# Optimization experiments

Hardware: AMD Instinct MI355X
Metric: run time of the kernel (lower is better)

The kernel has to match this reference:

```python
import jax, jax.numpy as jnp
import numpy as np

N_E = 16384
E_DIM = 256


def setup_inputs() -> dict:
    key = jax.random.key(0)
    k1, k2 = jax.random.split(key)
    z = jax.random.normal(k1, (16, E_DIM, 32, 32), dtype=jnp.float32)
    # nn.Embedding init: uniform(-1/n_e, 1/n_e)
    embedding_weight = jax.random.uniform(
        k2, (N_E, E_DIM), dtype=jnp.float32, minval=-1.0 / N_E, maxval=1.0 / N_E
    )
    return {"z": z, "embedding_weight": embedding_weight}


def reference(z, embedding_weight):
    # b c h w -> b h w c, flatten to (N, e_dim)
    zf = jnp.transpose(z, (0, 2, 3, 1)).reshape(-1, E_DIM)  # [N, d]
    # squared euclidean distances: ||z||^2 + ||e||^2 - 2 z.e^T
    d = (
        jnp.sum(zf ** 2, axis=1, keepdims=True)          # [N, 1]
        + jnp.sum(embedding_weight ** 2, axis=1)         # [n_e]
        - 2.0 * jnp.einsum("bd,nd->bn", zf, embedding_weight)  # [N, n_e]
    )
    min_encoding_indices = jnp.argmin(d, axis=1)  # [N] int
    return min_encoding_indices
```

## Files before the change

kernel.cpp:

```cpp
#include <hip/hip_runtime.h>

#define EDIM 256
#define NROW 16384
#define NCODE 16384
#define NBN 128
#define MARGIN 2.0e-4f

typedef _Float16 f16x8 __attribute__((ext_vector_type(8)));
typedef float f32x4 __attribute__((ext_vector_type(4)));

__device__ __forceinline__ void gll16(const void* g, void* l) {
  __builtin_amdgcn_global_load_lds((const __attribute__((address_space(1))) void*)g,
                                   (__attribute__((address_space(3))) void*)l, 16, 0, 0);
}
__device__ __forceinline__ void gll4(const void* g, void* l) {
  __builtin_amdgcn_global_load_lds((const __attribute__((address_space(1))) void*)g,
                                   (__attribute__((address_space(3))) void*)l, 4, 0, 0);
}

__global__ __launch_bounds__(256) void k_es(const float* __restrict__ e,
                                            float* __restrict__ es) {
  const int row = blockIdx.x * 4 + (threadIdx.x >> 6);
  const int lane = threadIdx.x & 63;
  float4 v = *(const float4*)&e[row * EDIM + lane * 4];
  double s = (double)v.x * v.x + (double)v.y * v.y + (double)v.z * v.z + (double)v.w * v.w;
#pragma unroll
  for (int off = 32; off > 0; off >>= 1) s += __shfl_down(s, off, 64);
  if (lane == 0) es[row] = (float)s;
}

__global__ __launch_bounds__(256) void k_cvt_e(const float* __restrict__ e,
                                               _Float16* __restrict__ Eh) {
  const int n = blockIdx.x;
  Eh[n * EDIM + threadIdx.x] = (_Float16)(e[n * EDIM + threadIdx.x] * 1024.0f);
}

__global__ __launch_bounds__(256) void k_cvt_z(const float* __restrict__ z,
                                               _Float16* __restrict__ Zh) {
  __shared__ float zl[EDIM * 64];
  const int t = threadIdx.x;
  const int rb = blockIdx.x;
  const int bb = rb >> 4;
  const int hw0 = (rb & 15) << 6;
  const float* zbase = z + (size_t)bb * EDIM * 1024 + hw0;
#pragma unroll 4
  for (int rep = 0; rep < 64; ++rep) {
    int c = rep * 4 + (t >> 6);
    zl[c * 64 + (t & 63)] = zbase[(size_t)c * 1024 + (t & 63)];
  }
  __syncthreads();
  const int mloc = t >> 2, part = t & 3;
#pragma unroll
  for (int i = 0; i < 8; ++i) {
    int c0 = part * 64 + i * 8;
    f16x8 v;
#pragma unroll
    for (int j = 0; j < 8; ++j) v[j] = (_Float16)zl[(c0 + j) * 64 + mloc];
    *(f16x8*)&Zh[(size_t)(rb * 64 + mloc) * EDIM + c0] = v;
  }
}

__global__ __launch_bounds__(256, 2) void k_gemm(const _Float16* __restrict__ Zh,
                                                 const _Float16* __restrict__ Eh,
                                                 float* __restrict__ lmin,
                                                 uint4* __restrict__ masks) {
  __shared__ __align__(16) char smem[32768];

  const int tid = threadIdx.x;
  const int lane = tid & 63;
  const int wv = tid >> 6;
  const int wm = wv & 1, wn = wv >> 1;
  const int fr = lane & 15;
  const int fq = lane >> 4;

  const int bid = (int)blockIdx.x;
  const int wgid = (bid & 7) * 2048 + (bid >> 3);
  const int st = wgid >> 8, wi = wgid & 255;
  const int bm = ((st & 7) << 4) | (wi & 15);
  const int bn = ((st >> 3) << 4) | (wi >> 4);

  const char* zh_b = (const char*)Zh;
  const char* eh_b = (const char*)Eh;

  auto stage = [&](int buf, int s) {
#pragma unroll
    for (int i = 0; i < 2; ++i) {
      const int L = (i * 256 + tid) * 16;
      const int row = L >> 6, kb = L & 63;
      gll16(zh_b + (size_t)(bm * 128 + row) * 512 + s * 64 + kb,
            smem + buf * 8192 + L);
      gll16(eh_b + (size_t)(bn * 128 + row) * 512 + s * 64 + kb,
            smem + 16384 + buf * 8192 + L);
    }
  };

  f32x4 acc[4][4];
#pragma unroll
  for (int i = 0; i < 4; ++i)
#pragma unroll
    for (int j = 0; j < 4; ++j) acc[i][j] = (f32x4)0.0f;

  stage(0, 0);
  __syncthreads();
#pragma unroll 1
  for (int s = 0; s < 8; ++s) {
    if (s + 1 < 8) stage((s + 1) & 1, s + 1);
    const char* aB = smem + (s & 1) * 8192;
    const char* bB = smem + 16384 + (s & 1) * 8192;
    f16x8 af[4], bf[4];
#pragma unroll
    for (int mi = 0; mi < 4; ++mi)
      af[mi] = *(const f16x8*)(aB + (wm * 64 + mi * 16 + fr) * 64 + fq * 16);
#pragma unroll
    for (int ni = 0; ni < 4; ++ni)
      bf[ni] = *(const f16x8*)(bB + (wn * 64 + ni * 16 + fr) * 64 + fq * 16);
#pragma unroll
    for (int mi = 0; mi < 4; ++mi)
#pragma unroll
      for (int ni = 0; ni < 4; ++ni)
        acc[mi][ni] = __builtin_amdgcn_mfma_f32_16x16x32_f16(af[mi], bf[ni], acc[mi][ni], 0, 0, 0);
    __syncthreads();
  }

  float* rowsmin = (float*)smem;
  float* rowminC = (float*)(smem + 1024);
  unsigned* msk = (unsigned*)(smem + 1536);
  msk[tid] = 0;
  msk[tid + 256] = 0;
  const float sc = -0.001953125f;
#pragma unroll
  for (int mi = 0; mi < 4; ++mi)
#pragma unroll
    for (int r = 0; r < 4; ++r) {
      float v = acc[mi][0][r] * sc;
      v = fminf(v, acc[mi][1][r] * sc);
      v = fminf(v, acc[mi][2][r] * sc);
      v = fminf(v, acc[mi][3][r] * sc);
#pragma unroll
      for (int off = 1; off < 16; off <<= 1) v = fminf(v, __shfl_xor(v, off, 64));
      if (fr == 0) rowsmin[(wm * 64 + mi * 16 + fq * 4 + r) * 2 + wn] = v;
    }
  __syncthreads();
  if (tid < 128) {
    float rm = fminf(rowsmin[tid * 2], rowsmin[tid * 2 + 1]);
    rowminC[tid] = rm;
    lmin[(size_t)bn * NROW + bm * 128 + tid] = rm;
  }
  __syncthreads();
#pragma unroll
  for (int mi = 0; mi < 4; ++mi)
#pragma unroll
    for (int r = 0; r < 4; ++r) {
      const int row = wm * 64 + mi * 16 + fq * 4 + r;
      const float thr = rowminC[row] + MARGIN;
#pragma unroll
      for (int ni = 0; ni < 4; ++ni) {
        if (acc[mi][ni][r] * sc <= thr) {
          const int col = wn * 64 + ni * 16 + fr;
          atomicOr(&msk[row * 4 + (col >> 5)], 1u << (col & 31));
        }
      }
    }
  __syncthreads();
  if (tid < 128) masks[(size_t)bn * NROW + bm * 128 + tid] = *(const uint4*)&msk[tid * 4];
}

__global__ __launch_bounds__(256) void k_rescore(const float* __restrict__ z,
                                                 const float* __restrict__ e,
                                                 const float* __restrict__ es,
                                                 const float* __restrict__ lmin,
                                                 const uint4* __restrict__ masks,
                                                 int* __restrict__ out) {
  extern __shared__ float zl[];
  float* lmin_s = zl + EDIM * 64;
  const int t = threadIdx.x;
  const int rb = (int)blockIdx.x;
  const int bb = rb >> 4;
  const int hw0 = (rb & 15) << 6;
  const int r0 = rb * 64;
  const float* zbase = z + (size_t)bb * EDIM * 1024 + hw0;
#pragma unroll 4
  for (int rep = 0; rep < 64; ++rep) {
    int c = rep * 4 + (t >> 6);
    zl[c * 64 + (t & 63)] = zbase[(size_t)c * 1024 + (t & 63)];
  }
#pragma unroll 4
  for (int i = 0; i < 32; ++i) {
    int bn = i * 4 + (t >> 6);
    lmin_s[bn * 64 + (t & 63)] = lmin[(size_t)bn * NROW + r0 + (t & 63)];
  }
  __syncthreads();

  const int r = t >> 2, q = t & 3;
  const int row = r0 + r;

  double sq = 0.0;
  {
    const float* zq = zl + (q * 64) * 64 + r;
    for (int k = 0; k < 64; ++k) {
      float v = zq[k * 64];
      sq = fma((double)v, (double)v, sq);
    }
  }
  double s01 = sq + __shfl_xor(sq, 1, 64);
  double zsd = s01 + __shfl_xor(s01, 2, 64);
  const float zs = (float)zsd;

  float g = 3.402823466e+38f;
#pragma unroll 8
  for (int j = 0; j < 32; ++j) g = fminf(g, lmin_s[(q * 32 + j) * 64 + r]);
  g = fminf(g, __shfl_xor(g, 1, 64));
  g = fminf(g, __shfl_xor(g, 2, 64));
  const float thr = g + MARGIN;

  float bestd = 3.402823466e+38f;
  int besti = 0x7fffffff;
#pragma unroll 1
  for (int j = 0; j < 32; ++j) {
    const int bn = q * 32 + j;
    if (lmin_s[bn * 64 + r] <= thr) {
      uint4 mk = masks[(size_t)bn * NROW + row];
      unsigned w[4] = {mk.x, mk.y, mk.z, mk.w};
#pragma unroll 1
      for (int qq = 0; qq < 4; ++qq) {
        unsigned u = w[qq];
        while (u) {
          int b = __ffs(u) - 1;
          u &= u - 1;
          const int code = bn * 128 + qq * 32 + b;
          const float* ep = e + (size_t)code * EDIM;
          float dot = 0.0f;
          for (int k = 0; k < EDIM; k += 4) {
            float4 ev = *(const float4*)(ep + k);
            dot = fmaf(zl[(k + 0) * 64 + r], ev.x, dot);
            dot = fmaf(zl[(k + 1) * 64 + r], ev.y, dot);
            dot = fmaf(zl[(k + 2) * 64 + r], ev.z, dot);
            dot = fmaf(zl[(k + 3) * 64 + r], ev.w, dot);
          }
          float d = (zs + es[code]) - 2.0f * dot;
          if (d < bestd) {
            bestd = d;
            besti = code;
          }
        }
      }
    }
  }
#pragma unroll
  for (int off = 1; off <= 2; off <<= 1) {
    float ov = __shfl_xor(bestd, off, 64);
    int oi = __shfl_xor(besti, off, 64);
    if (ov < bestd || (ov == bestd && oi < besti)) {
      bestd = ov;
      besti = oi;
    }
  }
  if (q == 0) out[row] = besti;
}

__global__ __launch_bounds__(256) void k_merge(const float* __restrict__ candv,
                                               const int* __restrict__ candi,
                                               int* __restrict__ out) {
  int n = blockIdx.x * 256 + threadIdx.x;
  float v0 = candv[n], v1 = candv[NROW + n];
  int i0 = candi[n], i1 = candi[NROW + n];
  out[n] = (v1 < v0) ? i1 : i0;
}

template <int SPLIT>
__global__ __launch_bounds__(256, 2) void k_main_fb(const float* __restrict__ z,
                                                    const float* __restrict__ e,
                                                    const float* __restrict__ es,
                                                    float* __restrict__ candv,
                                                    int* __restrict__ candi,
                                                    int* __restrict__ outd) {
  extern __shared__ char smemc[];
  float* As = (float*)smemc;
  float* Bs = (float*)(smemc + 16384);
  double* zred = (double*)(smemc + 16384 + 32768);
  float* zsf = (float*)(smemc + 16384 + 32768 + 2048);
  const int tid = threadIdx.x;
  const int lane = tid & 63;
  const int wv = tid >> 6;
  const int tm = tid & 7;
  const int tn = tid >> 3;
  const int rt = (int)blockIdx.x / SPLIT;
  const int sp = (int)blockIdx.x % SPLIT;
  const int bb = rt >> 4;
  const int hw0 = (rt & 15) << 6;
  const float* zb = z + bb * (EDIM * 1024) + hw0;
  const int codeBase = sp * (NCODE / SPLIT);
  const int NSTEP = (NCODE / SPLIT) / 256 * 8;
  auto stageA = [&](int buf, int gts) {
    const int k0 = (gts & 7) * 32;
    const float* g0 = zb + (size_t)k0 * 1024 + lane;
    float* l0 = As + buf * 2048 + (wv * 8) * 64;
#pragma unroll
    for (int s = 0; s < 8; ++s) gll4(g0 + (size_t)(wv * 8 + s) * 1024, l0 + s * 64);
  };
  float4 bpre[8];
  auto loadB = [&](int gts) {
    const int ct = gts >> 3, k0 = (gts & 7) * 32;
    const float* g = e + (size_t)(codeBase + ct * 256 + tid) * 256 + k0;
#pragma unroll
    for (int s = 0; s < 8; ++s) bpre[s] = *(const float4*)(g + s * 4);
  };
  auto writeB = [&](int buf) {
    float* bw_ = Bs + buf * 8192 + tid;
#pragma unroll
    for (int s = 0; s < 8; ++s) {
      bw_[(4 * s + 0) * 256] = bpre[s].x;
      bw_[(4 * s + 1) * 256] = bpre[s].y;
      bw_[(4 * s + 2) * 256] = bpre[s].z;
      bw_[(4 * s + 3) * 256] = bpre[s].w;
    }
  };
  stageA(0, 0);
  loadB(0);
  {
    const int m = tid & 63, qt = tid >> 6;
    const float* zp = zb + (size_t)(qt * 64) * 1024 + m;
    double s = 0.0;
    for (int k = 0; k < 64; ++k) {
      float v = zp[(size_t)k * 1024];
      s = fma((double)v, (double)v, s);
    }
    zred[qt * 64 + m] = s;
  }
  writeB(0);
  __syncthreads();
  if (tid < 64) {
    double sz = (zred[tid] + zred[64 + tid]) + (zred[128 + tid] + zred[192 + tid]);
    zsf[tid] = (float)sz;
  }
  __syncthreads();
  float zsr[8];
#pragma unroll
  for (int i = 0; i < 8; ++i) zsr[i] = zsf[tm * 8 + i];
  __syncthreads();
  float bestv[8];
  int besti[8];
#pragma unroll
  for (int i = 0; i < 8; ++i) {
    bestv[i] = 3.402823466e+38f;
    besti[i] = 0;
  }
  float acc[8][8];
  int cur = 0;
#pragma unroll 1
  for (int step = 0; step < NSTEP; ++step) {
    const int kc = step & 7, ct = step >> 3;
    if (step + 1 < NSTEP) {
      stageA(cur ^ 1, step + 1);
      loadB(step + 1);
    }
    if (kc == 0) {
#pragma unroll
      for (int i = 0; i < 8; ++i)
#pragma unroll
        for (int j = 0; j < 8; ++j) acc[i][j] = 0.0f;
    }
    const float* ak = As + cur * 2048 + tm * 8;
    const float* bk = Bs + cur * 8192 + tn * 8;
#pragma unroll 4
    for (int k = 0; k < 32; ++k) {
      float4 a0 = *(const float4*)(ak + k * 64);
      float4 a1 = *(const float4*)(ak + k * 64 + 4);
      float4 b0 = *(const float4*)(bk + k * 256);
      float4 b1 = *(const float4*)(bk + k * 256 + 4);
      float av[8] = {a0.x, a0.y, a0.z, a0.w, a1.x, a1.y, a1.z, a1.w};
      float bw[8] = {b0.x, b0.y, b0.z, b0.w, b1.x, b1.y, b1.z, b1.w};
#pragma unroll
      for (int i = 0; i < 8; ++i)
#pragma unroll
        for (int j = 0; j < 8; ++j) acc[i][j] = fmaf(av[i], bw[j], acc[i][j]);
    }
    if (step + 1 < NSTEP) writeB(cur ^ 1);
    if (kc == 7) {
      const int cb = codeBase + ct * 256 + tn * 8;
#pragma unroll
      for (int j = 0; j < 8; ++j) {
        float ej = es[cb + j];
#pragma unroll
        for (int i = 0; i < 8; ++i) {
          float d = (zsr[i] + ej) - 2.0f * acc[i][j];
          if (d < bestv[i]) {
            bestv[i] = d;
            besti[i] = cb + j;
          }
        }
      }
    }
    __syncthreads();
    cur ^= 1;
  }
  float* Lv = (float*)(smemc + 16384);
  int* Li = (int*)(smemc + 16384 + 8192);
#pragma unroll
  for (int i = 0; i < 8; ++i) {
    Lv[(tm * 8 + i) * 32 + tn] = bestv[i];
    Li[(tm * 8 + i) * 32 + tn] = besti[i];
  }
  __syncthreads();
  if (tid < 64) {
    float bv = Lv[tid * 32];
    int bi = Li[tid * 32];
#pragma unroll 1
    for (int g2 = 1; g2 < 32; ++g2) {
      float v = Lv[tid * 32 + g2];
      int ii = Li[tid * 32 + g2];
      if (v < bv || (v == bv && ii < bi)) {
        bv = v;
        bi = ii;
      }
    }
    if (SPLIT == 1) outd[rt * 64 + tid] = bi;
    else {
      candv[sp * NROW + rt * 64 + tid] = bv;
      candi[sp * NROW + rt * 64 + tid] = bi;
    }
  }
}

extern "C" void kernel_launch(void* const* d_in, const int* in_sizes, int n_in,
                              void* d_out, int out_size, void* d_ws, size_t ws_size,
                              hipStream_t stream) {
  const float* z = (const float*)d_in[0];
  const float* e = (const float*)d_in[1];
  int* out = (int*)d_out;

  char* ws = (char*)d_ws;
  float* es = (float*)ws;
  const size_t off_zh = 65536;
  const size_t off_eh = off_zh + (size_t)NROW * EDIM * 2;
  const size_t off_lmin = off_eh + (size_t)NCODE * EDIM * 2;
  const size_t off_masks = off_lmin + (size_t)NROW * NBN * 4;
  const size_t need = off_masks + (size_t)NROW * NBN * 16;

  k_es<<<dim3(NCODE / 4), dim3(256), 0, stream>>>(e, es);

  if (ws_size >= need) {
    _Float16* Zh = (_Float16*)(ws + off_zh);
    _Float16* Eh = (_Float16*)(ws + off_eh);
    float* lmin = (float*)(ws + off_lmin);
    uint4* masks = (uint4*)(ws + off_masks);
    k_cvt_e<<<dim3(NCODE), dim3(256), 0, stream>>>(e, Eh);
    k_cvt_z<<<dim3(256), dim3(256), 0, stream>>>(z, Zh);
    k_gemm<<<dim3(16384), dim3(256), 0, stream>>>(Zh, Eh, lmin, masks);
    hipFuncSetAttribute(reinterpret_cast<const void*>(&k_rescore),
                        hipFuncAttributeMaxDynamicSharedMemorySize, 98304);
    k_rescore<<<dim3(256), dim3(256), 98304, stream>>>(z, e, es, lmin, masks, out);
  } else {
    float* candv = (float*)(ws + 65536);
    int* candi = (int*)(ws + 65536 + 131072);
    const size_t smem = 16384 + 65536;
    if (ws_size >= 65536 + 131072 + 131072) {
      hipFuncSetAttribute(reinterpret_cast<const void*>(&k_main_fb<2>),
                          hipFuncAttributeMaxDynamicSharedMemorySize, (int)smem);
      k_main_fb<2><<<dim3(512), dim3(256), smem, stream>>>(z, e, es, candv, candi, out);
      k_merge<<<dim3(NROW / 256), dim3(256), 0, stream>>>(candv, candi, out);
    } else {
      hipFuncSetAttribute(reinterpret_cast<const void*>(&k_main_fb<1>),
                          hipFuncAttributeMaxDynamicSharedMemorySize, (int)smem);
      k_main_fb<1><<<dim3(256), dim3(256), smem, stream>>>(z, e, es, candv, candi, out);
    }
  }
}
```

Before: 417.6 us.

## Enlarge GEMM M-tile to 256, swizzle LDS, use ballot masks, fuse E prep

The GEMM tile grows from 128x128 to 256x128 rows per block, halving the grid and improving reuse of the E tile. The LDS layout gets an XOR swizzle to reduce bank conflicts on fragment reads. Candidate mask building switches from per-element LDS atomicOr to wave ballots. The E norm and fp16 conversion kernels are merged into one launch. The larger accumulator array (128 floats per thread) raises register pressure under launch_bounds(256,2), which may cause spills or lower occupancy.

Result: slower. 476.7 us (+14.2%).

```diff
diff --git a/kernel.cpp b/kernel.cpp
--- a/kernel.cpp
+++ b/kernel.cpp
@@ -7,6 +7,7 @@
 #define MARGIN 2.0e-4f
 
 typedef _Float16 f16x8 __attribute__((ext_vector_type(8)));
+typedef _Float16 f16x4 __attribute__((ext_vector_type(4)));
 typedef float f32x4 __attribute__((ext_vector_type(4)));
 
 __device__ __forceinline__ void gll16(const void* g, void* l) {
@@ -16,6 +17,24 @@
 __device__ __forceinline__ void gll4(const void* g, void* l) {
   __builtin_amdgcn_global_load_lds((const __attribute__((address_space(1))) void*)g,
                                    (__attribute__((address_space(3))) void*)l, 4, 0, 0);
+}
+
+__global__ __launch_bounds__(256) void k_prep_e(const float* __restrict__ e,
+                                                float* __restrict__ es,
+                                                _Float16* __restrict__ Eh) {
+  const int row = blockIdx.x * 4 + (threadIdx.x >> 6);
+  const int lane = threadIdx.x & 63;
+  float4 v = *(const float4*)&e[row * EDIM + lane * 4];
+  f16x4 h;
+  h[0] = (_Float16)(v.x * 1024.0f);
+  h[1] = (_Float16)(v.y * 1024.0f);
+  h[2] = (_Float16)(v.z * 1024.0f);
+  h[3] = (_Float16)(v.w * 1024.0f);
+  *(f16x4*)&Eh[row * EDIM + lane * 4] = h;
+  double s = (double)v.x * v.x + (double)v.y * v.y + (double)v.z * v.z + (double)v.w * v.w;
+#pragma unroll
+  for (int off = 32; off > 0; off >>= 1) s += __shfl_down(s, off, 64);
+  if (lane == 0) es[row] = (float)s;
 }
 
 __global__ __launch_bounds__(256) void k_es(const float* __restrict__ e,
@@ -27,12 +46,6 @@
 #pragma unroll
   for (int off = 32; off > 0; off >>= 1) s += __shfl_down(s, off, 64);
   if (lane == 0) es[row] = (float)s;
-}
-
-__global__ __launch_bounds__(256) void k_cvt_e(const float* __restrict__ e,
-                                               _Float16* __restrict__ Eh) {
-  const int n = blockIdx.x;
-  Eh[n * EDIM + threadIdx.x] = (_Float16)(e[n * EDIM + threadIdx.x] * 1024.0f);
 }
 
 __global__ __launch_bounds__(256) void k_cvt_z(const float* __restrict__ z,
@@ -64,7 +77,9 @@
                                                  const _Float16* __restrict__ Eh,
                                                  float* __restrict__ lmin,
                                                  uint4* __restrict__ masks) {
-  __shared__ __align__(16) char smem[32768];
+  __shared__ __align__(16) char smem[49152];
+  char* smemA = smem;
+  char* smemB = smem + 32768;
 
   const int tid = threadIdx.x;
   const int lane = tid & 63;
@@ -72,31 +87,37 @@
   const int wm = wv & 1, wn = wv >> 1;
   const int fr = lane & 15;
   const int fq = lane >> 4;
+  const int swz = (fq ^ ((fr >> 1) & 3)) * 16;
 
   const int bid = (int)blockIdx.x;
-  const int wgid = (bid & 7) * 2048 + (bid >> 3);
-  const int st = wgid >> 8, wi = wgid & 255;
-  const int bm = ((st & 7) << 4) | (wi & 15);
-  const int bn = ((st >> 3) << 4) | (wi >> 4);
+  const int wgid = (bid & 7) * 1024 + (bid >> 3);
+  const int st = wgid >> 7, wi = wgid & 127;
+  const int bm = ((st & 7) << 3) | (wi & 7);
+  const int bn = ((st >> 3) << 4) | (wi >> 3);
 
   const char* zh_b = (const char*)Zh;
   const char* eh_b = (const char*)Eh;
 
   auto stage = [&](int buf, int s) {
 #pragma unroll
+    for (int i = 0; i < 4; ++i) {
+      const int L = (i * 256 + tid) * 16;
+      const int row = L >> 6, p = (L >> 4) & 3;
+      gll16(zh_b + (size_t)(bm * 256 + row) * 512 + s * 64 + ((p ^ ((row >> 1) & 3)) * 16),
+            smemA + buf * 16384 + L);
+    }
+#pragma unroll
     for (int i = 0; i < 2; ++i) {
       const int L = (i * 256 + tid) * 16;
-      const int row = L >> 6, kb = L & 63;
-      gll16(zh_b + (size_t)(bm * 128 + row) * 512 + s * 64 + kb,
-            smem + buf * 8192 + L);
-      gll16(eh_b + (size_t)(bn * 128 + row) * 512 + s * 64 + kb,
-            smem + 16384 + buf * 8192 + L);
+      const int row = L >> 6, p = (L >> 4) & 3;
+      gll16(eh_b + (size_t)(bn * 128 + row) * 512 + s * 64 + ((p ^ ((row >> 1) & 3)) * 16),
+            smemB + buf * 8192 + L);
     }
   };
 
-  f32x4 acc[4][4];
-#pragma unroll
-  for (int i = 0; i < 4; ++i)
+  f32x4 acc[8][4];
+#pragma unroll
+  for (int i = 0; i < 8; ++i)
 #pragma unroll
     for (int j = 0; j < 4; ++j) acc[i][j] = (f32x4)0.0f;
 
@@ -105,17 +126,17 @@
 #pragma unroll 1
   for (int s = 0; s < 8; ++s) {
     if (s + 1 < 8) stage((s + 1) & 1, s + 1);
-    const char* aB = smem + (s & 1) * 8192;
-    const char* bB = smem + 16384 + (s & 1) * 8192;
-    f16x8 af[4], bf[4];
-#pragma unroll
-    for (int mi = 0; mi < 4; ++mi)
-      af[mi] = *(const f16x8*)(aB + (wm * 64 + mi * 16 + fr) * 64 + fq * 16);
+    const char* aB = smemA + (s & 1) * 16384;
+    const char* bB = smemB + (s & 1) * 8192;
+    f16x8 af[8], bf[4];
+#pragma unroll
+    for (int mi = 0; mi < 8; ++mi)
+      af[mi] = *(const f16x8*)(aB + (wm * 128 + mi * 16 + fr) * 64 + swz);
 #pragma unroll
     for (int ni = 0; ni < 4; ++ni)
-      bf[ni] = *(const f16x8*)(bB + (wn * 64 + ni * 16 + fr) * 64 + fq * 16);
-#pragma unroll
-    for (int mi = 0; mi < 4; ++mi)
+      bf[ni] = *(const f16x8*)(bB + (wn * 64 + ni * 16 + fr) * 64 + swz);
+#pragma unroll
+    for (int mi = 0; mi < 8; ++mi)
 #pragma unroll
       for (int ni = 0; ni < 4; ++ni)
         acc[mi][ni] = __builtin_amdgcn_mfma_f32_16x16x32_f16(af[mi], bf[ni], acc[mi][ni], 0, 0, 0);
@@ -123,13 +144,11 @@
   }
 
   float* rowsmin = (float*)smem;
-  float* rowminC = (float*)(smem + 1024);
-  unsigned* msk = (unsigned*)(smem + 1536);
-  msk[tid] = 0;
-  msk[tid + 256] = 0;
+  float* rowminC = (float*)(smem + 2048);
+  unsigned short* msk16 = (unsigned short*)(smem + 3072);
   const float sc = -0.001953125f;
 #pragma unroll
-  for (int mi = 0; mi < 4; ++mi)
+  for (int mi = 0; mi < 8; ++mi)
 #pragma unroll
     for (int r = 0; r < 4; ++r) {
       float v = acc[mi][0][r] * sc;
@@ -138,31 +157,30 @@
       v = fminf(v, acc[mi][3][r] * sc);
 #pragma unroll
       for (int off = 1; off < 16; off <<= 1) v = fminf(v, __shfl_xor(v, off, 64));
-      if (fr == 0) rowsmin[(wm * 64 + mi * 16 + fq * 4 + r) * 2 + wn] = v;
-    }
-  __syncthreads();
-  if (tid < 128) {
+      if (fr == 0) rowsmin[(wm * 128 + mi * 16 + fq * 4 + r) * 2 + wn] = v;
+    }
+  __syncthreads();
+  if (tid < 256) {
     float rm = fminf(rowsmin[tid * 2], rowsmin[tid * 2 + 1]);
     rowminC[tid] = rm;
-    lmin[(size_t)bn * NROW + bm * 128 + tid] = rm;
-  }
-  __syncthreads();
-#pragma unroll
-  for (int mi = 0; mi < 4; ++mi)
+    lmin[(size_t)bn * NROW + bm * 256 + tid] = rm;
+  }
+  __syncthreads();
+#pragma unroll
+  for (int mi = 0; mi < 8; ++mi)
 #pragma unroll
     for (int r = 0; r < 4; ++r) {
-      const int row = wm * 64 + mi * 16 + fq * 4 + r;
+      const int row = wm * 128 + mi * 16 + fq * 4 + r;
       const float thr = rowminC[row] + MARGIN;
 #pragma unroll
       for (int ni = 0; ni < 4; ++ni) {
-        if (acc[mi][ni][r] * sc <= thr) {
-          const int col = wn * 64 + ni * 16 + fr;
-          atomicOr(&msk[row * 4 + (col >> 5)], 1u << (col & 31));
-        }
+        unsigned long long bal = __ballot(acc[mi][ni][r] * sc <= thr);
+        if (fr == 0) msk16[row * 8 + wn * 4 + ni] = (unsigned short)((bal >> (fq * 16)) & 0xffffull);
       }
     }
   __syncthreads();
-  if (tid < 128) masks[(size_t)bn * NROW + bm * 128 + tid] = *(const uint4*)&msk[tid * 4];
+  if (tid < 256)
+    masks[(size_t)bn * NROW + bm * 256 + tid] = *(const uint4*)&msk16[tid * 8];
 }
 
 __global__ __launch_bounds__(256) void k_rescore(const float* __restrict__ z,
@@ -437,20 +455,19 @@
   const size_t off_masks = off_lmin + (size_t)NROW * NBN * 4;
   const size_t need = off_masks + (size_t)NROW * NBN * 16;
 
-  k_es<<<dim3(NCODE / 4), dim3(256), 0, stream>>>(e, es);
-
   if (ws_size >= need) {
     _Float16* Zh = (_Float16*)(ws + off_zh);
     _Float16* Eh = (_Float16*)(ws + off_eh);
     float* lmin = (float*)(ws + off_lmin);
     uint4* masks = (uint4*)(ws + off_masks);
-    k_cvt_e<<<dim3(NCODE), dim3(256), 0, stream>>>(e, Eh);
+    k_prep_e<<<dim3(NCODE / 4), dim3(256), 0, stream>>>(e, es, Eh);
     k_cvt_z<<<dim3(256), dim3(256), 0, stream>>>(z, Zh);
-    k_gemm<<<dim3(16384), dim3(256), 0, stream>>>(Zh, Eh, lmin, masks);
+    k_gemm<<<dim3(8192), dim3(256), 0, stream>>>(Zh, Eh, lmin, masks);
     hipFuncSetAttribute(reinterpret_cast<const void*>(&k_rescore),
                         hipFuncAttributeMaxDynamicSharedMemorySize, 98304);
     k_rescore<<<dim3(256), dim3(256), 98304, stream>>>(z, e, es, lmin, masks, out);
   } else {
+    k_es<<<dim3(NCODE / 4), dim3(256), 0, stream>>>(e, es);
     float* candv = (float*)(ws + 65536);
     int* candi = (int*)(ws + 65536 + 131072);
     const size_t smem = 16384 + 65536;
```

## Swizzle GEMM LDS tiles, ballot-based candidate masks, fuse E prep kernels

Applied to the files above, without the earlier changes.

Applies an XOR swizzle to the 16-byte chunks of each 64-byte LDS row in the fp16 GEMM, in both the global-to-LDS staging and the fragment reads, to cut LDS bank conflicts. The candidate-mask construction drops shared-memory atomicOr in favour of wave ballots, writing 16-bit mask pieces directly, which also removes the mask zeroing. The code-norm and fp16 conversion kernels for the embedding table are merged into one pass with vectorized stores, saving a launch and a read of the table. The changes add index arithmetic, and the ballot path relies on the fq/fr lane mapping matching the MFMA output layout.

Result: faster. 407.7 us (-2.4%).

```diff
diff --git a/kernel.cpp b/kernel.cpp
--- a/kernel.cpp
+++ b/kernel.cpp
@@ -7,6 +7,7 @@
 #define MARGIN 2.0e-4f
 
 typedef _Float16 f16x8 __attribute__((ext_vector_type(8)));
+typedef _Float16 f16x4 __attribute__((ext_vector_type(4)));
 typedef float f32x4 __attribute__((ext_vector_type(4)));
 
 __device__ __forceinline__ void gll16(const void* g, void* l) {
@@ -16,6 +17,24 @@
 __device__ __forceinline__ void gll4(const void* g, void* l) {
   __builtin_amdgcn_global_load_lds((const __attribute__((address_space(1))) void*)g,
                                    (__attribute__((address_space(3))) void*)l, 4, 0, 0);
+}
+
+__global__ __launch_bounds__(256) void k_prep_e(const float* __restrict__ e,
+                                                float* __restrict__ es,
+                                                _Float16* __restrict__ Eh) {
+  const int row = blockIdx.x * 4 + (threadIdx.x >> 6);
+  const int lane = threadIdx.x & 63;
+  float4 v = *(const float4*)&e[row * EDIM + lane * 4];
+  f16x4 h;
+  h[0] = (_Float16)(v.x * 1024.0f);
+  h[1] = (_Float16)(v.y * 1024.0f);
+  h[2] = (_Float16)(v.z * 1024.0f);
+  h[3] = (_Float16)(v.w * 1024.0f);
+  *(f16x4*)&Eh[row * EDIM + lane * 4] = h;
+  double s = (double)v.x * v.x + (double)v.y * v.y + (double)v.z * v.z + (double)v.w * v.w;
+#pragma unroll
+  for (int off = 32; off > 0; off >>= 1) s += __shfl_down(s, off, 64);
+  if (lane == 0) es[row] = (float)s;
 }
 
 __global__ __launch_bounds__(256) void k_es(const float* __restrict__ e,
@@ -27,12 +46,6 @@
 #pragma unroll
   for (int off = 32; off > 0; off >>= 1) s += __shfl_down(s, off, 64);
   if (lane == 0) es[row] = (float)s;
-}
-
-__global__ __launch_bounds__(256) void k_cvt_e(const float* __restrict__ e,
-                                               _Float16* __restrict__ Eh) {
-  const int n = blockIdx.x;
-  Eh[n * EDIM + threadIdx.x] = (_Float16)(e[n * EDIM + threadIdx.x] * 1024.0f);
 }
 
 __global__ __launch_bounds__(256) void k_cvt_z(const float* __restrict__ z,
@@ -65,6 +78,8 @@
                                                  float* __restrict__ lmin,
                                                  uint4* __restrict__ masks) {
   __shared__ __align__(16) char smem[32768];
+  char* smemA = smem;
+  char* smemB = smem + 16384;
 
   const int tid = threadIdx.x;
   const int lane = tid & 63;
@@ -72,6 +87,7 @@
   const int wm = wv & 1, wn = wv >> 1;
   const int fr = lane & 15;
   const int fq = lane >> 4;
+  const int swz = (fq ^ ((fr >> 1) & 3)) * 16;
 
   const int bid = (int)blockIdx.x;
   const int wgid = (bid & 7) * 2048 + (bid >> 3);
@@ -86,11 +102,10 @@
 #pragma unroll
     for (int i = 0; i < 2; ++i) {
       const int L = (i * 256 + tid) * 16;
-      const int row = L >> 6, kb = L & 63;
-      gll16(zh_b + (size_t)(bm * 128 + row) * 512 + s * 64 + kb,
-            smem + buf * 8192 + L);
-      gll16(eh_b + (size_t)(bn * 128 + row) * 512 + s * 64 + kb,
-            smem + 16384 + buf * 8192 + L);
+      const int row = L >> 6, p = (L >> 4) & 3;
+      const int gsw = (p ^ ((row >> 1) & 3)) * 16;
+      gll16(zh_b + (size_t)(bm * 128 + row) * 512 + s * 64 + gsw, smemA + buf * 8192 + L);
+      gll16(eh_b + (size_t)(bn * 128 + row) * 512 + s * 64 + gsw, smemB + buf * 8192 + L);
     }
   };
 
@@ -105,15 +120,15 @@
 #pragma unroll 1
   for (int s = 0; s < 8; ++s) {
     if (s + 1 < 8) stage((s + 1) & 1, s + 1);
-    const char* aB = smem + (s & 1) * 8192;
-    const char* bB = smem + 16384 + (s & 1) * 8192;
+    const char* aB = smemA + (s & 1) * 8192;
+    const char* bB = smemB + (s & 1) * 8192;
     f16x8 af[4], bf[4];
 #pragma unroll
     for (int mi = 0; mi < 4; ++mi)
-      af[mi] = *(const f16x8*)(aB + (wm * 64 + mi * 16 + fr) * 64 + fq * 16);
+      af[mi] = *(const f16x8*)(aB + (wm * 64 + mi * 16 + fr) * 64 + swz);
 #pragma unroll
     for (int ni = 0; ni < 4; ++ni)
-      bf[ni] = *(const f16x8*)(bB + (wn * 64 + ni * 16 + fr) * 64 + fq * 16);
+      bf[ni] = *(const f16x8*)(bB + (wn * 64 + ni * 16 + fr) * 64 + swz);
 #pragma unroll
     for (int mi = 0; mi < 4; ++mi)
 #pragma unroll
@@ -124,9 +139,7 @@
 
   float* rowsmin = (float*)smem;
   float* rowminC = (float*)(smem + 1024);
-  unsigned* msk = (unsigned*)(smem + 1536);
-  msk[tid] = 0;
-  msk[tid + 256] = 0;
+  unsigned short* msk16 = (unsigned short*)(smem + 1536);
   const float sc = -0.001953125f;
 #pragma unroll
   for (int mi = 0; mi < 4; ++mi)
@@ -155,14 +168,13 @@
       const float thr = rowminC[row] + MARGIN;
 #pragma unroll
       for (int ni = 0; ni < 4; ++ni) {
-        if (acc[mi][ni][r] * sc <= thr) {
-          const int col = wn * 64 + ni * 16 + fr;
-          atomicOr(&msk[row * 4 + (col >> 5)], 1u << (col & 31));
-        }
+        unsigned long long bal = __ballot(acc[mi][ni][r] * sc <= thr);
+        if (fr == 0) msk16[row * 8 + wn * 4 + ni] = (unsigned short)((bal >> (fq * 16)) & 0xffffull);
       }
     }
   __syncthreads();
-  if (tid < 128) masks[(size_t)bn * NROW + bm * 128 + tid] = *(const uint4*)&msk[tid * 4];
+  if (tid < 128)
+    masks[(size_t)bn * NROW + bm * 128 + tid] = *(const uint4*)&msk16[tid * 8];
 }
 
 __global__ __launch_bounds__(256) void k_rescore(const float* __restrict__ z,
@@ -437,20 +449,19 @@
   const size_t off_masks = off_lmin + (size_t)NROW * NBN * 4;
   const size_t need = off_masks + (size_t)NROW * NBN * 16;
 
-  k_es<<<dim3(NCODE / 4), dim3(256), 0, stream>>>(e, es);
-
   if (ws_size >= need) {
     _Float16* Zh = (_Float16*)(ws + off_zh);
     _Float16* Eh = (_Float16*)(ws + off_eh);
     float* lmin = (float*)(ws + off_lmin);
     uint4* masks = (uint4*)(ws + off_masks);
-    k_cvt_e<<<dim3(NCODE), dim3(256), 0, stream>>>(e, Eh);
+    k_prep_e<<<dim3(NCODE / 4), dim3(256), 0, stream>>>(e, es, Eh);
     k_cvt_z<<<dim3(256), dim3(256), 0, stream>>>(z, Zh);
     k_gemm<<<dim3(16384), dim3(256), 0, stream>>>(Zh, Eh, lmin, masks);
     hipFuncSetAttribute(reinterpret_cast<const void*>(&k_rescore),
                         hipFuncAttributeMaxDynamicSharedMemorySize, 98304);
     k_rescore<<<dim3(256), dim3(256), 98304, stream>>>(z, e, es, lmin, masks, out);
   } else {
+    k_es<<<dim3(NCODE / 4), dim3(256), 0, stream>>>(e, es);
     float* candv = (float*)(ws + 65536);
     int* candi = (int*)(ws + 65536 + 131072);
     const size_t smem = 16384 + 65536;
```
